# Kernel optimization log

Hardware: AMD Instinct MI355X
Metric: run time of the kernel (lower is better)

## Reference

```python
import jax, jax.numpy as jnp
import numpy as np

B, C, H, W = 2, 64, 512, 896


def setup_inputs() -> dict:
    key = jax.random.key(0)
    k1, k2 = jax.random.split(key)
    feature = jax.random.normal(k1, (B, C, H, W), dtype=jnp.float32)
    # flow in pixel units; a few pixels of motion is typical for video frames
    flow = jax.random.normal(k2, (B, 2, H, W), dtype=jnp.float32) * 3.0
    return {"feature": feature, "flow": flow}


def reference(feature, flow):
    # Flownet2-style Resample2d: out[b,c,y,x] = bilinear(feature[b,c], y+v, x+u)
    # with zero contribution from out-of-bounds taps.
    Bv, Cv, Hv, Wv = feature.shape
    HW = Hv * Wv
    gx = flow[:, 0] + jnp.arange(Wv, dtype=flow.dtype)[None, None, :]  # [B,H,W]
    gy = flow[:, 1] + jnp.arange(Hv, dtype=flow.dtype)[None, :, None]  # [B,H,W]
    x0f = jnp.floor(gx)
    y0f = jnp.floor(gy)
    wx = gx - x0f  # frac weights
    wy = gy - y0f
    x0 = x0f.astype(jnp.int32)
    y0 = y0f.astype(jnp.int32)
    feat = feature.reshape(Bv, Cv, HW)

    def corner(xi, yi, w):
        # zero out-of-bounds taps; clip indices so the gather is always legal
        valid = (xi >= 0) & (xi < Wv) & (yi >= 0) & (yi < Hv)
        idx = jnp.clip(yi, 0, Hv - 1) * Wv + jnp.clip(xi, 0, Wv - 1)  # [B,H,W]
        idx = jnp.broadcast_to(idx.reshape(Bv, 1, HW), (Bv, Cv, HW))
        v = jnp.take_along_axis(feat, idx, axis=2)  # [B,C,HW]
        wm = (w * valid.astype(w.dtype)).reshape(Bv, 1, HW)
        return v * wm

    out = (
        corner(x0, y0, (1.0 - wx) * (1.0 - wy))
        + corner(x0 + 1, y0, wx * (1.0 - wy))
        + corner(x0, y0 + 1, (1.0 - wx) * wy)
        + corner(x0 + 1, y0 + 1, wx * wy)
    )
    return out.reshape(Bv, Cv, Hv, Wv)
```

## Files before the change

### kernel.cpp

```cpp
#include <hip/hip_runtime.h>


#define Bv 2
#define Cv 64
#define Hv 512
#define Wv 896
#define HWsz (Hv * Wv)

#define TILE 64
#define CPB 2
#define GPB 4
#define NCG (Cv / CPB)
#define NCGB (NCG / GPB)
#define SW 91
#define SH 88
#define XOFF 12
#define YOFF 11
#define NSITES (SH * SW)
#define NTX (Wv / TILE)
#define NTY (Hv / TILE)
#define NTILES (NTX * NTY)
#define NBLK (Bv * NCGB * NTILES)
#define THREADS 1024
#define NW (THREADS / 64)
#define KITERS (TILE * TILE / THREADS)
#define SITE_ITERS ((NSITES + THREADS - 1) / THREADS)
#define LDS_BYTES (2 * NSITES * (int)sizeof(float2))

__global__ __launch_bounds__(THREADS, 4) void resample2d_kernel(
    const float* __restrict__ feature,
    const float* __restrict__ flow,
    float* __restrict__ out) {
    extern __shared__ float2 smem[];
    float2* const buf0 = smem;
    float2* const buf1 = smem + NSITES;

    const int orig = blockIdx.x;
    const int wid = (orig & 7) * (NBLK / 8) + (orig >> 3);
    const int txi = wid % NTX;
    const int t2 = wid / NTX;
    const int tyi = t2 % NTY;
    const int zb = t2 / NTY;
    const int b = zb / NCGB;
    const int c0 = (zb % NCGB) * (GPB * CPB);

    const int tx0 = txi * TILE;
    const int ty0 = tyi * TILE;
    const int xs = tx0 - XOFF;
    const int ys = ty0 - YOFF;

    const int tid = threadIdx.x;
    const int lane = tid & 63;
    const int wv = tid >> 6;

    const float* __restrict__ fbase = feature + ((size_t)b * Cv + c0) * HWsz;
    const float* __restrict__ flb = flow + (size_t)b * 2 * HWsz;
    float* __restrict__ ob = out + ((size_t)b * Cv + c0) * HWsz;

    const int px = tx0 + lane;
    float u[KITERS], v[KITERS];
    int pixk[KITERS];
#pragma unroll
    for (int k = 0; k < KITERS; ++k) {
        const int y = ty0 + wv + NW * k;
        pixk[k] = y * Wv + px;
        u[k] = flb[pixk[k]];
        v[k] = flb[HWsz + pixk[k]];
    }

    int sOff[SITE_ITERS];
    int gOff[SITE_ITERS];
    float vmask[SITE_ITERS];
#pragma unroll
    for (int i = 0; i < SITE_ITERS; ++i) {
        const int p = tid + THREADS * i;
        const int pc = (p < NSITES) ? p : (NSITES - 1);
        const int r = pc / SW;
        const int xx = pc - r * SW;
        const int gy = ys + r;
        const int gx = xs + xx;
        const bool vd = ((unsigned)gy < (unsigned)Hv) & ((unsigned)gx < (unsigned)Wv);
        gOff[i] = vd ? (gy * Wv + gx) : 0;
        vmask[i] = vd ? 1.0f : 0.0f;
        sOff[i] = pc;
    }

#define STAGE_LOAD(G)                                            \
    do {                                                         \
        const float* __restrict__ fg_ =                          \
            fbase + (size_t)(G) * CPB * HWsz;                    \
        _Pragma("unroll") for (int i = 0; i < SITE_ITERS; ++i) { \
            a0[i] = fg_[gOff[i]];                                \
            a1[i] = fg_[gOff[i] + HWsz];                         \
        }                                                        \
    } while (0)

#define STAGE_WRITE(BUF)                                                   \
    do {                                                                   \
        _Pragma("unroll") for (int i = 0; i < SITE_ITERS; ++i) {           \
            BUF[sOff[i]] = make_float2(a0[i] * vmask[i], a1[i] * vmask[i]); \
        }                                                                  \
    } while (0)

    float a0[SITE_ITERS], a1[SITE_ITERS];
    STAGE_LOAD(0);

    float w00k[KITERS], w10k[KITERS], w01k[KITERS], w11k[KITERS];
    int ac[KITERS];
    unsigned iw = 0;
#pragma unroll
    for (int k = 0; k < KITERS; ++k) {
        const int y = ty0 + wv + NW * k;
        const float gx = u[k] + (float)px;
        const float gy = v[k] + (float)y;
        const float x0f = floorf(gx);
        const float y0f = floorf(gy);
        const float wx = gx - x0f;
        const float wy = gy - y0f;
        const float omx = 1.0f - wx;
        const float omy = 1.0f - wy;
        w00k[k] = omx * omy;
        w10k[k] = wx * omy;
        w01k[k] = omx * wy;
        w11k[k] = wx * wy;
        const int lx = (int)x0f - xs;
        const int ly = (int)y0f - ys;
        const bool inwin = ((unsigned)lx <= (unsigned)(SW - 2)) &
                           ((unsigned)ly <= (unsigned)(SH - 2));
        iw |= inwin ? (1u << k) : 0u;
        const int lxc = min(max(lx, 0), SW - 2);
        const int lyc = min(max(ly, 0), SH - 2);
        ac[k] = lyc * SW + lxc;
    }

#define COMPUTE(G, BUF)                                                        \
    do {                                                                       \
        float* __restrict__ og_ = ob + (size_t)(G) * CPB * HWsz;               \
        const float* __restrict__ fg_ = fbase + (size_t)(G) * CPB * HWsz;      \
        _Pragma("unroll") for (int k = 0; k < KITERS; ++k) {                   \
            float2 t00 = BUF[ac[k]];                                           \
            float2 t10 = BUF[ac[k] + 1];                                       \
            float2 t01 = BUF[ac[k] + SW];                                      \
            float2 t11 = BUF[ac[k] + SW + 1];                                  \
            if (!(iw & (1u << k))) {          \
                const int y_ = ty0 + wv + NW * k;                              \
                const float gx_ = u[k] + (float)px;                            \
                const float gy_ = v[k] + (float)y_;                            \
                const int x0_ = (int)floorf(gx_);                              \
                const int y0_ = (int)floorf(gy_);                              \
                const int x1_ = x0_ + 1, y1_ = y0_ + 1;                        \
                const bool vx0 = (unsigned)x0_ < (unsigned)Wv;                 \
                const bool vx1 = (unsigned)x1_ < (unsigned)Wv;                 \
                const bool vy0 = (unsigned)y0_ < (unsigned)Hv;                 \
                const bool vy1 = (unsigned)y1_ < (unsigned)Hv;                 \
                const int cx0 = min(max(x0_, 0), Wv - 1);                      \
                const int cx1 = min(max(x1_, 0), Wv - 1);                      \
                const int cy0 = min(max(y0_, 0), Hv - 1);                      \
                const int cy1 = min(max(y1_, 0), Hv - 1);                      \
                _Pragma("unroll") for (int c = 0; c < CPB; ++c) {              \
                    const float* f = fg_ + (size_t)c * HWsz;                   \
                    ((float*)&t00)[c] = (vx0 & vy0) ? f[cy0 * Wv + cx0] : 0.f; \
                    ((float*)&t10)[c] = (vx1 & vy0) ? f[cy0 * Wv + cx1] : 0.f; \
                    ((float*)&t01)[c] = (vx0 & vy1) ? f[cy1 * Wv + cx0] : 0.f; \
                    ((float*)&t11)[c] = (vx1 & vy1) ? f[cy1 * Wv + cx1] : 0.f; \
                }                                                              \
            }                                                                  \
            const float r0 = t00.x * w00k[k] + t10.x * w10k[k] +               \
                             t01.x * w01k[k] + t11.x * w11k[k];                \
            const float r1 = t00.y * w00k[k] + t10.y * w10k[k] +               \
                             t01.y * w01k[k] + t11.y * w11k[k];                \
            __builtin_nontemporal_store(r0, &og_[pixk[k]]);                    \
            __builtin_nontemporal_store(r1, &og_[HWsz + pixk[k]]);             \
        }                                                                      \
    } while (0)

    STAGE_WRITE(buf0);
    __syncthreads();

    STAGE_LOAD(1);
    COMPUTE(0, buf0);
    STAGE_WRITE(buf1);
    __syncthreads();

    STAGE_LOAD(2);
    COMPUTE(1, buf1);
    STAGE_WRITE(buf0);
    __syncthreads();

    STAGE_LOAD(3);
    COMPUTE(2, buf0);
    STAGE_WRITE(buf1);
    __syncthreads();

    COMPUTE(3, buf1);

#undef STAGE_LOAD
#undef STAGE_WRITE
#undef COMPUTE
}

extern "C" void kernel_launch(void* const* d_in, const int* in_sizes, int n_in,
                              void* d_out, int out_size, void* d_ws, size_t ws_size,
                              hipStream_t stream) {
    const float* feature = (const float*)d_in[0];
    const float* flow = (const float*)d_in[1];
    float* out = (float*)d_out;

    static bool inited = false;
    if (!inited) {
        hipFuncSetAttribute((const void*)resample2d_kernel,
                            hipFuncAttributeMaxDynamicSharedMemorySize, LDS_BYTES);
        inited = true;
    }

    dim3 block(THREADS, 1, 1);
    dim3 grid(NBLK, 1, 1);
    resample2d_kernel<<<grid, block, LDS_BYTES, stream>>>(feature, flow, out);
}
```

Baseline: 425.3 us.

## Single-buffer the LDS halo and cut registers to double block occupancy

Replaces the double-buffered LDS halo (two buffers of NSITES float2 each) with a single static buffer, adding an extra barrier before each refill. Per-site LDS offsets, float masks and output pixel indices are now recomputed or packed into a bitmask instead of held in registers. Launch bounds rise from 4 to 8 blocks per CU. The aim is higher occupancy to hide gather latency, at the cost of an extra synchronisation per channel group and the loss of overlap between LDS writes and reads.

Result: slower. 621.7 us (+46.2%).

```diff
diff --git a/kernel.cpp b/kernel.cpp
--- a/kernel.cpp
+++ b/kernel.cpp
@@ -25,15 +25,12 @@
 #define NW (THREADS / 64)
 #define KITERS (TILE * TILE / THREADS)
 #define SITE_ITERS ((NSITES + THREADS - 1) / THREADS)
-#define LDS_BYTES (2 * NSITES * (int)sizeof(float2))
-
-__global__ __launch_bounds__(THREADS, 4) void resample2d_kernel(
+
+__global__ __launch_bounds__(THREADS, 8) void resample2d_kernel(
     const float* __restrict__ feature,
     const float* __restrict__ flow,
     float* __restrict__ out) {
-    extern __shared__ float2 smem[];
-    float2* const buf0 = smem;
-    float2* const buf1 = smem + NSITES;
+    __shared__ float2 smem[NSITES];
 
     const int orig = blockIdx.x;
     const int wid = (orig & 7) * (NBLK / 8) + (orig >> 3);
@@ -59,18 +56,15 @@
 
     const int px = tx0 + lane;
     float u[KITERS], v[KITERS];
-    int pixk[KITERS];
 #pragma unroll
     for (int k = 0; k < KITERS; ++k) {
-        const int y = ty0 + wv + NW * k;
-        pixk[k] = y * Wv + px;
-        u[k] = flb[pixk[k]];
-        v[k] = flb[HWsz + pixk[k]];
+        const int pix = (ty0 + wv + NW * k) * Wv + px;
+        u[k] = flb[pix];
+        v[k] = flb[HWsz + pix];
     }
 
-    int sOff[SITE_ITERS];
     int gOff[SITE_ITERS];
-    float vmask[SITE_ITERS];
+    unsigned vbits = 0;
 #pragma unroll
     for (int i = 0; i < SITE_ITERS; ++i) {
         const int p = tid + THREADS * i;
@@ -81,8 +75,7 @@
         const int gx = xs + xx;
         const bool vd = ((unsigned)gy < (unsigned)Hv) & ((unsigned)gx < (unsigned)Wv);
         gOff[i] = vd ? (gy * Wv + gx) : 0;
-        vmask[i] = vd ? 1.0f : 0.0f;
-        sOff[i] = pc;
+        vbits |= vd ? (1u << i) : 0u;
     }
 
 #define STAGE_LOAD(G)                                            \
@@ -95,11 +88,14 @@
         }                                                        \
     } while (0)
 
-#define STAGE_WRITE(BUF)                                                   \
-    do {                                                                   \
-        _Pragma("unroll") for (int i = 0; i < SITE_ITERS; ++i) {           \
-            BUF[sOff[i]] = make_float2(a0[i] * vmask[i], a1[i] * vmask[i]); \
-        }                                                                  \
+#define STAGE_WRITE()                                                       \
+    do {                                                                    \
+        _Pragma("unroll") for (int i = 0; i < SITE_ITERS; ++i) {            \
+            const int p_ = tid + THREADS * i;                               \
+            const int pc_ = (p_ < NSITES) ? p_ : (NSITES - 1);              \
+            const float m_ = (vbits & (1u << i)) ? 1.0f : 0.0f;             \
+            smem[pc_] = make_float2(a0[i] * m_, a1[i] * m_);                \
+        }                                                                   \
     } while (0)
 
     float a0[SITE_ITERS], a1[SITE_ITERS];
@@ -133,15 +129,15 @@
         ac[k] = lyc * SW + lxc;
     }
 
-#define COMPUTE(G, BUF)                                                        \
+#define COMPUTE(G)                                                             \
     do {                                                                       \
         float* __restrict__ og_ = ob + (size_t)(G) * CPB * HWsz;               \
         const float* __restrict__ fg_ = fbase + (size_t)(G) * CPB * HWsz;      \
         _Pragma("unroll") for (int k = 0; k < KITERS; ++k) {                   \
-            float2 t00 = BUF[ac[k]];                                           \
-            float2 t10 = BUF[ac[k] + 1];                                       \
-            float2 t01 = BUF[ac[k] + SW];                                      \
-            float2 t11 = BUF[ac[k] + SW + 1];                                  \
+            float2 t00 = smem[ac[k]];                                          \
+            float2 t10 = smem[ac[k] + 1];                                      \
+            float2 t01 = smem[ac[k] + SW];                                     \
+            float2 t11 = smem[ac[k] + SW + 1];                                 \
             if (!(iw & (1u << k))) {          \
                 const int y_ = ty0 + wv + NW * k;                              \
                 const float gx_ = u[k] + (float)px;                            \
@@ -169,30 +165,34 @@
                              t01.x * w01k[k] + t11.x * w11k[k];                \
             const float r1 = t00.y * w00k[k] + t10.y * w10k[k] +               \
                              t01.y * w01k[k] + t11.y * w11k[k];                \
-            __builtin_nontemporal_store(r0, &og_[pixk[k]]);                    \
-            __builtin_nontemporal_store(r1, &og_[HWsz + pixk[k]]);             \
+            const int pix_ = (ty0 + wv + NW * k) * Wv + px;                    \
+            __builtin_nontemporal_store(r0, &og_[pix_]);                       \
+            __builtin_nontemporal_store(r1, &og_[HWsz + pix_]);                \
         }                                                                      \
     } while (0)
 
-    STAGE_WRITE(buf0);
+    STAGE_WRITE();
     __syncthreads();
 
     STAGE_LOAD(1);
-    COMPUTE(0, buf0);
-    STAGE_WRITE(buf1);
+    COMPUTE(0);
+    __syncthreads();
+    STAGE_WRITE();
     __syncthreads();
 
     STAGE_LOAD(2);
-    COMPUTE(1, buf1);
-    STAGE_WRITE(buf0);
+    COMPUTE(1);
+    __syncthreads();
+    STAGE_WRITE();
     __syncthreads();
 
     STAGE_LOAD(3);
-    COMPUTE(2, buf0);
-    STAGE_WRITE(buf1);
-    __syncthreads();
-
-    COMPUTE(3, buf1);
+    COMPUTE(2);
+    __syncthreads();
+    STAGE_WRITE();
+    __syncthreads();
+
+    COMPUTE(3);
 
 #undef STAGE_LOAD
 #undef STAGE_WRITE
@@ -206,14 +206,7 @@
     const float* flow = (const float*)d_in[1];
     float* out = (float*)d_out;
 
-    static bool inited = false;
-    if (!inited) {
-        hipFuncSetAttribute((const void*)resample2d_kernel,
-                            hipFuncAttributeMaxDynamicSharedMemorySize, LDS_BYTES);
-        inited = true;
-    }
-
     dim3 block(THREADS, 1, 1);
     dim3 grid(NBLK, 1, 1);
-    resample2d_kernel<<<grid, block, LDS_BYTES, stream>>>(feature, flow, out);
+    resample2d_kernel<<<grid, block, 0, stream>>>(feature, flow, out);
 }
```
